# Kernel tuning notes

Hardware: AMD Instinct MI355X
Metric: run time of the kernel (lower is better)

## Reference

```python
import jax, jax.numpy as jnp
import numpy as np

B, D, C, H, L = 32768, 64, 64, 1024, 6
EPS = 1e-5
NIN = (D - D // 2) + C  # unchanged half + cond = 96
SPLIT = D // 2          # 32


def setup_inputs() -> dict:
    key = jax.random.key(0)
    ks = jax.random.split(key, 12)
    s = 0.05
    return {
        "z": jax.random.normal(ks[0], (B, D), jnp.float32),
        "cond": jax.random.normal(ks[1], (B, C), jnp.float32),
        "W1": jax.random.normal(ks[2], (L, NIN, H), jnp.float32) * s,
        "b1": jax.random.normal(ks[3], (L, H), jnp.float32) * s,
        "W2": jax.random.normal(ks[4], (L, H, H), jnp.float32) * s,
        "b2": jax.random.normal(ks[5], (L, H), jnp.float32) * s,
        "Ws": jax.random.normal(ks[6], (L, H, SPLIT), jnp.float32) * s,
        "bs": jax.random.normal(ks[7], (L, SPLIT), jnp.float32) * s,
        "Wt": jax.random.normal(ks[8], (L, H, SPLIT), jnp.float32) * s,
        "bt": jax.random.normal(ks[9], (L, SPLIT), jnp.float32) * s,
        "bn_w": 1.0 + 0.1 * jax.random.normal(ks[10], (L, D), jnp.float32),
        "bn_b": 0.1 * jax.random.normal(ks[11], (L, D), jnp.float32),
    }


def reference(z, cond, W1, b1, W2, b2, Ws, bs, Wt, bt, bn_w, bn_b):
    x = z
    log_det = jnp.zeros((z.shape[0],), z.dtype)
    for i in range(L):
        # 'even' mask keeps even indices on even layers, odd indices otherwise
        if i % 2 == 0:
            keep, chg = np.arange(0, D, 2), np.arange(1, D, 2)
        else:
            keep, chg = np.arange(1, D, 2), np.arange(0, D, 2)
        # 2-layer MLP on [x_keep, cond]
        h = jax.nn.relu(jnp.concatenate([x[:, keep], cond], axis=1) @ W1[i] + b1[i])
        h = jax.nn.relu(h @ W2[i] + b2[i])
        log_s = jnp.tanh(h @ Ws[i] + bs[i])          # (B, SPLIT)
        t = h @ Wt[i] + bt[i]                         # (B, SPLIT)
        x2t = x[:, chg] * jnp.exp(log_s) + t
        x = jnp.zeros_like(x).at[:, keep].set(x[:, keep]).at[:, chg].set(x2t)
        log_det = log_det + log_s.sum(axis=1)
        # BatchNorm1d, training mode: batch mean / biased variance, eps=1e-5
        mean = x.mean(axis=0)
        var = x.var(axis=0)
        x = (x - mean) * jax.lax.rsqrt(var + EPS) * bn_w[i] + bn_b[i]
        log_det = log_det + jnp.log(jnp.abs(bn_w[i])).sum()
    return x, log_det
```

## Files before the change

kernel.cpp:

```cpp
#include <hip/hip_runtime.h>
#include <math.h>

#define BB 32768
#define DD 64
#define CC 64
#define HH 1024
#define LL 6
#define SPLIT 32
#define NIN 96
#define EPSV 1e-5f

typedef short short8 __attribute__((ext_vector_type(8)));
typedef float f32x4 __attribute__((ext_vector_type(4)));
typedef unsigned short u16;

__device__ __forceinline__ u16 f2bf(float f) {
    union { float f; unsigned int u; } c; c.f = f;
    unsigned int u = c.u + 0x7FFFu + ((c.u >> 16) & 1u);
    return (u16)(u >> 16);
}

__device__ __forceinline__ void gl_lds16(const u16* g, u16* l) {
    __builtin_amdgcn_global_load_lds(
        (const __attribute__((address_space(1))) unsigned int*)g,
        (__attribute__((address_space(3))) unsigned int*)l, 16, 0, 0);
}

__global__ void transpose_cvt_kernel(const float* __restrict__ src, u16* __restrict__ dst,
                                     int R, int C, int Rpad,
                                     long long sstride, long long dstride)
{
    __shared__ float tile[32][33];
    const float* s = src + (size_t)blockIdx.z * sstride;
    u16* d = dst + (size_t)blockIdx.z * dstride;
    int r0 = blockIdx.x * 32, c0 = blockIdx.y * 32;
    int tc = threadIdx.x & 31, tr = threadIdx.x >> 5;
#pragma unroll
    for (int i = 0; i < 4; ++i) {
        int r = r0 + tr + i * 8;
        tile[tr + i * 8][tc] = (r < R) ? s[(size_t)r * C + c0 + tc] : 0.f;
    }
    __syncthreads();
#pragma unroll
    for (int i = 0; i < 4; ++i) {
        int cc = tr + i * 8;
        d[(size_t)(c0 + cc) * Rpad + r0 + tc] = f2bf(tile[tc][cc]);
    }
}

__global__ __launch_bounds__(256)
void init_ain_cond_kernel(const float* __restrict__ cond, u16* __restrict__ Ain)
{
    int t = blockIdx.x * 256 + threadIdx.x;
    int c = t % 96, r = t / 96;
    Ain[(size_t)r * 128 + 32 + c] = (c < CC) ? f2bf(cond[(size_t)r * CC + c]) : (u16)0;
}

__global__ __launch_bounds__(256)
void build_keep_kernel(const float* __restrict__ x, u16* __restrict__ Ain, int keep_off)
{
    int t = blockIdx.x * 256 + threadIdx.x;
    int c = t & 31, r = t >> 5;
    Ain[(size_t)r * 128 + c] = f2bf(x[(size_t)r * DD + 2 * c + keep_off]);
}

__global__ __launch_bounds__(512, 4)
void gemm_tiled(const u16* __restrict__ A,
                const u16* __restrict__ Bt,
                const float* __restrict__ bias,
                u16* __restrict__ Cc,
                int K)
{
    __shared__ u16 sA[3][8 * 512];
    __shared__ u16 sB[3][16 * 512];

    const int t = threadIdx.x;
    const int w = t >> 6, lane = t & 63;
    const int lane16 = lane & 15, quad = lane >> 4;
    const int wm = w >> 2, wn = w & 3;

    int id = blockIdx.x;
    int nby = gridDim.x >> 2;
    int xcd = id & 7, slot = id >> 3;
    int bx = slot & 3, byq = slot >> 2;
    int by = xcd * (nby >> 3) + byq;
    const int bm = by * 128, bn = bx * 256;

    const int niter = K >> 5;

    auto stage = [&](int it, int buf) {
        int k0 = it * 32;
#pragma unroll
        for (int e3 = 0; e3 < 3; ++e3) {
            int e = w + e3 * 8;
            if (e < 8) {
                const u16* g = A + (size_t)(bm + e * 16 + lane16) * K + k0 + quad * 8;
                gl_lds16(g, &sA[buf][e * 512]);
            } else {
                int j = e - 8;
                const u16* g = Bt + (size_t)(bn + j * 16 + lane16) * K + k0 + quad * 8;
                gl_lds16(g, &sB[buf][j * 512]);
            }
        }
    };

    f32x4 acc[4][4];
#pragma unroll
    for (int a = 0; a < 4; ++a)
#pragma unroll
        for (int b = 0; b < 4; ++b) acc[a][b] = (f32x4){0.f, 0.f, 0.f, 0.f};

    const unsigned sAb = (unsigned)(size_t)(__attribute__((address_space(3))) u16*)&sA[0][0];
    const unsigned sBb = (unsigned)(size_t)(__attribute__((address_space(3))) u16*)&sB[0][0];
    const unsigned aoff = (unsigned)(wm * 4096 + lane * 16);
    const unsigned boff = (unsigned)(wn * 4096 + lane * 16);

    stage(0, 0);
    stage(1, 1);
    int buf = 0, sbuf = 2;
    for (int it = 0; it < niter; ++it) {
        asm volatile("s_waitcnt vmcnt(3)");
        __builtin_amdgcn_s_barrier();

        const unsigned aA = sAb + (unsigned)(buf * 8192)  + aoff;
        const unsigned aB = sBb + (unsigned)(buf * 16384) + boff;
        short8 af0, af1, af2, af3, bf0, bf1, bf2, bf3;
        asm volatile("ds_read_b128 %0, %1 offset:0"    : "=v"(af0) : "v"(aA));
        asm volatile("ds_read_b128 %0, %1 offset:1024" : "=v"(af1) : "v"(aA));
        asm volatile("ds_read_b128 %0, %1 offset:2048" : "=v"(af2) : "v"(aA));
        asm volatile("ds_read_b128 %0, %1 offset:3072" : "=v"(af3) : "v"(aA));
        asm volatile("ds_read_b128 %0, %1 offset:0"    : "=v"(bf0) : "v"(aB));
        asm volatile("ds_read_b128 %0, %1 offset:1024" : "=v"(bf1) : "v"(aB));
        asm volatile("ds_read_b128 %0, %1 offset:2048" : "=v"(bf2) : "v"(aB));
        asm volatile("ds_read_b128 %0, %1 offset:3072" : "=v"(bf3) : "v"(aB));

        if (it + 2 < niter)        stage(it + 2, sbuf);
        else if (it + 2 == niter)  stage(niter - 1, sbuf);

        asm volatile("s_waitcnt lgkmcnt(0)");
        __builtin_amdgcn_sched_barrier(0);

        short8 af[4] = {af0, af1, af2, af3};
        short8 bfr[4] = {bf0, bf1, bf2, bf3};
#pragma unroll
        for (int a = 0; a < 4; ++a)
#pragma unroll
            for (int b = 0; b < 4; ++b)
                acc[a][b] = __builtin_amdgcn_mfma_f32_16x16x32_bf16(af[a], bfr[b], acc[a][b], 0, 0, 0);

        buf  = (buf  == 2) ? 0 : buf  + 1;
        sbuf = (sbuf == 2) ? 0 : sbuf + 1;
    }
    __syncthreads();

    constexpr int ES = 72;
    float bv[4];
#pragma unroll
    for (int b = 0; b < 4; ++b) bv[b] = bias[bn + wn * 64 + b * 16 + lane16];
    u16* scr = ((u16*)sB) + w * (16 * ES);
#pragma unroll
    for (int a = 0; a < 4; ++a) {
#pragma unroll
        for (int b = 0; b < 4; ++b)
#pragma unroll
            for (int r = 0; r < 4; ++r) {
                float v = fmaxf(acc[a][b][r] + bv[b], 0.f);
                scr[(quad * 4 + r) * ES + b * 16 + lane16] = f2bf(v);
            }
#pragma unroll
        for (int ch = 0; ch < 2; ++ch) {
            int row = ch * 8 + (lane >> 3), colc = (lane & 7) * 8;
            short8 v = *(const short8*)(scr + row * ES + colc);
            *(short8*)(Cc + (size_t)(bm + wm * 64 + a * 16 + row) * 1024 + bn + wn * 64 + colc) = v;
        }
    }
}

__global__ __launch_bounds__(512)
void gemm3_coupling(const u16* __restrict__ A,
                    const u16* __restrict__ Bt,
                    const float* __restrict__ bs, const float* __restrict__ bt,
                    float* __restrict__ x, float* __restrict__ log_det,
                    float* __restrict__ stat_sum, float* __restrict__ stat_sumsq,
                    int keep_off, int row0)
{
    constexpr int ST_STRIDE = 66;
    __shared__ u16 stg[2][24 * 512];
    __shared__ float ssum[8][64], ssum2[8][64];
    float* sst = (float*)stg;

    const int t = threadIdx.x;
    const int w = t >> 6, lane = t & 63;
    const int lane16 = lane & 15, quad = lane >> 4;
    const int wm = w >> 1, wn = w & 1;
    const int bm = blockIdx.x * 128;

    auto stage = [&](int it, int buf) {
        int k0 = it * 64;
#pragma unroll
        for (int p = 0; p < 3; ++p) {
            int e = w + p * 8;
            if (e < 16) {
                int s = e >> 3, i = e & 7;
                const u16* g = A + (size_t)(bm + i * 16 + lane16) * HH + (k0 + s * 32 + quad * 8);
                gl_lds16(g, &stg[buf][e * 512]);
            } else {
                int j2 = e - 16, s = j2 >> 2, j = j2 & 3;
                const u16* g = Bt + (size_t)(j * 16 + lane16) * HH + (k0 + s * 32 + quad * 8);
                gl_lds16(g, &stg[buf][e * 512]);
            }
        }
    };

    f32x4 acc[2][2];
#pragma unroll
    for (int a = 0; a < 2; ++a)
#pragma unroll
        for (int b = 0; b < 2; ++b) acc[a][b] = (f32x4){0.f, 0.f, 0.f, 0.f};

    stage(0, 0);
    for (int it = 0; it < 16; ++it) {
        const int buf = it & 1;
        __syncthreads();
        if (it + 1 < 16) stage(it + 1, buf ^ 1);
        u16* ldsA = stg[buf];
        u16* ldsB = stg[buf] + 16 * 512;
#pragma unroll
        for (int s = 0; s < 2; ++s) {
            short8 af[2], bfr[2];
#pragma unroll
            for (int a = 0; a < 2; ++a)
                af[a] = *(const short8*)(ldsA + ((s * 8 + wm * 2 + a) * 512) + lane * 8);
#pragma unroll
            for (int b = 0; b < 2; ++b)
                bfr[b] = *(const short8*)(ldsB + ((s * 4 + wn * 2 + b) * 512) + lane * 8);
#pragma unroll
            for (int a = 0; a < 2; ++a)
#pragma unroll
                for (int b = 0; b < 2; ++b)
                    acc[a][b] = __builtin_amdgcn_mfma_f32_16x16x32_bf16(af[a], bfr[b], acc[a][b], 0, 0, 0);
        }
    }
    __syncthreads();

#pragma unroll
    for (int a = 0; a < 2; ++a)
#pragma unroll
        for (int b = 0; b < 2; ++b)
#pragma unroll
            for (int r = 0; r < 4; ++r) {
                int row = wm * 32 + a * 16 + quad * 4 + r;
                int col = wn * 32 + b * 16 + lane16;
                sst[row * ST_STRIDE + col] = acc[a][b][r];
            }
    __syncthreads();

    const int f = lane;
    const bool is_chg = ((f & 1) != keep_off);
    const int j = f >> 1;
    float bsj = 0.f, btj = 0.f;
    if (is_chg) { bsj = bs[j]; btj = bt[j]; }

    float lsum = 0.f, lsum2 = 0.f;
    for (int i = 0; i < 16; ++i) {
        int crow = w * 16 + i;
        int grow = row0 + bm + crow;
        float xv = x[(size_t)grow * DD + f];
        float ld = 0.f;
        if (is_chg) {
            float s_raw = sst[crow * ST_STRIDE + j];
            float t_raw = sst[crow * ST_STRIDE + SPLIT + j];
            float ls = tanhf(s_raw + bsj);
            float tv = t_raw + btj;
            xv = xv * expf(ls) + tv;
            x[(size_t)grow * DD + f] = xv;
            ld = ls;
        }
        for (int off = 32; off > 0; off >>= 1) ld += __shfl_down(ld, off, 64);
        if (f == 0) log_det[grow] += ld;
        lsum  += xv;
        lsum2 += xv * xv;
    }

    ssum[w][f]  = lsum;
    ssum2[w][f] = lsum2;
    __syncthreads();
    if (t < 64) {
        float a = 0.f, b = 0.f;
#pragma unroll
        for (int g = 0; g < 8; ++g) { a += ssum[g][t]; b += ssum2[g][t]; }
        atomicAdd(stat_sum + t, a);
        atomicAdd(stat_sumsq + t, b);
    }
}

__global__ __launch_bounds__(256)
void normalize_kernel(const float* __restrict__ xin, float* __restrict__ xout,
                      const float* __restrict__ stat_sum, const float* __restrict__ stat_sumsq,
                      const float* __restrict__ bn_w, const float* __restrict__ bn_b,
                      float* __restrict__ log_det,
                      u16* __restrict__ Ain, int off_next)
{
    __shared__ float sscale[64], sshift[64], scsum;
    int t = threadIdx.x;
    if (t < 64) {
        const float invB = 1.f / (float)BB;
        float mean = stat_sum[t] * invB;
        float var  = stat_sumsq[t] * invB - mean * mean;
        float inv  = rsqrtf(var + EPSV);
        float wv   = bn_w[t];
        float sc   = inv * wv;
        sscale[t] = sc;
        sshift[t] = bn_b[t] - mean * sc;
        float lg = logf(fabsf(wv));
        for (int off = 32; off > 0; off >>= 1) lg += __shfl_down(lg, off, 64);
        if (t == 0) scsum = lg;
    }
    __syncthreads();

    int idx = blockIdx.x * blockDim.x + t;
    int f0 = (idx & 15) * 4;
    int row = idx >> 4;
    float4 v = ((const float4*)xin)[idx];
    v.x = v.x * sscale[f0 + 0] + sshift[f0 + 0];
    v.y = v.y * sscale[f0 + 1] + sshift[f0 + 1];
    v.z = v.z * sscale[f0 + 2] + sshift[f0 + 2];
    v.w = v.w * sscale[f0 + 3] + sshift[f0 + 3];
    ((float4*)xout)[idx] = v;
    if ((idx & 15) == 0) log_det[row] += scsum;
    if (Ain) {
        float a0 = off_next ? v.y : v.x;
        float a1 = off_next ? v.w : v.z;
        ushort2 u; u.x = f2bf(a0); u.y = f2bf(a1);
        *(ushort2*)(Ain + (size_t)row * 128 + (f0 >> 1)) = u;
    }
}

extern "C" void kernel_launch(void* const* d_in, const int* in_sizes, int n_in,
                              void* d_out, int out_size, void* d_ws, size_t ws_size,
                              hipStream_t stream)
{
    const float* z    = (const float*)d_in[0];
    const float* cond = (const float*)d_in[1];
    const float* W1   = (const float*)d_in[2];
    const float* b1   = (const float*)d_in[3];
    const float* W2   = (const float*)d_in[4];
    const float* b2   = (const float*)d_in[5];
    const float* Ws   = (const float*)d_in[6];
    const float* bs   = (const float*)d_in[7];
    const float* Wt   = (const float*)d_in[8];
    const float* bt   = (const float*)d_in[9];
    const float* bn_w = (const float*)d_in[10];
    const float* bn_b = (const float*)d_in[11];

    float* out_x  = (float*)d_out;
    float* out_ld = out_x + (size_t)BB * DD;

    char* p = (char*)d_ws;
    size_t used = 0;
    auto alloc = [&](size_t bytes) { void* q = p + used; used += (bytes + 255) & ~(size_t)255; return q; };

    float* xbuf = (float*)alloc((size_t)BB * DD * 4);
    u16*   w1t  = (u16*)alloc((size_t)LL * HH * 128 * 2);
    u16*   w2t  = (u16*)alloc((size_t)LL * HH * HH * 2);
    u16*   wstt = (u16*)alloc((size_t)LL * 64 * HH * 2);
    u16*   Ain  = (u16*)alloc((size_t)BB * 128 * 2);
    float* stat_sum   = (float*)alloc(64 * 4);
    float* stat_sumsq = (float*)alloc(64 * 4);

    int CH = BB;
    while (CH > 8192 && used + (size_t)CH * 4096 + 4096 > ws_size) CH >>= 1;
    u16* h1 = (u16*)alloc((size_t)CH * HH * 2);
    u16* h2 = (u16*)alloc((size_t)CH * HH * 2);

    hipMemcpyAsync(xbuf, z, (size_t)BB * DD * sizeof(float), hipMemcpyDeviceToDevice, stream);
    hipMemsetAsync(out_ld, 0, (size_t)BB * sizeof(float), stream);

    transpose_cvt_kernel<<<dim3(128/32, HH/32, LL), 256, 0, stream>>>(
        W1, w1t, NIN, HH, 128, (long long)NIN * HH, (long long)HH * 128);
    transpose_cvt_kernel<<<dim3(HH/32, HH/32, LL), 256, 0, stream>>>(
        W2, w2t, HH, HH, HH, (long long)HH * HH, (long long)HH * HH);
    transpose_cvt_kernel<<<dim3(HH/32, SPLIT/32, LL), 256, 0, stream>>>(
        Ws, wstt, HH, SPLIT, HH, (long long)HH * SPLIT, (long long)64 * HH);
    transpose_cvt_kernel<<<dim3(HH/32, SPLIT/32, LL), 256, 0, stream>>>(
        Wt, wstt + (size_t)SPLIT * HH, HH, SPLIT, HH, (long long)HH * SPLIT, (long long)64 * HH);

    init_ain_cond_kernel<<<BB * 96 / 256, 256, 0, stream>>>(cond, Ain);
    build_keep_kernel<<<BB * 32 / 256, 256, 0, stream>>>(xbuf, Ain, 0);

    for (int l = 0; l < LL; ++l) {
        const int off = l & 1;
        hipMemsetAsync(stat_sum, 0, 2 * 64 * sizeof(float), stream);

        for (int c = 0; c < BB / CH; ++c) {
            const int row0 = c * CH;

            gemm_tiled<<<(CH / 128) * 4, 512, 0, stream>>>(
                Ain + (size_t)row0 * 128, w1t + (size_t)l * HH * 128,
                b1 + (size_t)l * HH, h1, 128);

            gemm_tiled<<<(CH / 128) * 4, 512, 0, stream>>>(
                h1, w2t + (size_t)l * HH * HH,
                b2 + (size_t)l * HH, h2, HH);

            gemm3_coupling<<<CH / 128, 512, 0, stream>>>(
                h2, wstt + (size_t)l * 64 * HH,
                bs + (size_t)l * SPLIT, bt + (size_t)l * SPLIT,
                xbuf, out_ld, stat_sum, stat_sumsq, off, row0);
        }

        float* xout = (l == LL - 1) ? out_x : xbuf;
        u16* ain_next = (l < LL - 1) ? Ain : nullptr;
        normalize_kernel<<<(BB * DD / 4) / 256, 256, 0, stream>>>(
            xbuf, xout, stat_sum, stat_sumsq,
            bn_w + (size_t)l * DD, bn_b + (size_t)l * DD,
            out_ld, ain_next, (l + 1) & 1);
    }
}
```

Measured before the change: 1.088 ms.

## Enlarge GEMM block tile to 256x256 and split MFMA issue around LDS reads

The main bf16 GEMM block tile grows from 128x256 to 256x256, so each wave computes a 128x64 sub-tile with 32 accumulators, which raises the arithmetic done per staged A/B byte. The K-loop now waits for only the first half of its LDS fragment reads before issuing half of the MFMAs, and raises wave priority around the MFMA bursts. The cost is higher register and LDS use, with launch bounds lowered to 2 blocks per CU, and half as many blocks per chunk, which may leave CUs underused when chunks are small.

```diff
diff --git a/kernel.cpp b/kernel.cpp
--- a/kernel.cpp
+++ b/kernel.cpp
@@ -64,14 +64,14 @@
     Ain[(size_t)r * 128 + c] = f2bf(x[(size_t)r * DD + 2 * c + keep_off]);
 }
 
-__global__ __launch_bounds__(512, 4)
+__global__ __launch_bounds__(512, 2)
 void gemm_tiled(const u16* __restrict__ A,
                 const u16* __restrict__ Bt,
                 const float* __restrict__ bias,
                 u16* __restrict__ Cc,
                 int K)
 {
-    __shared__ u16 sA[3][8 * 512];
+    __shared__ u16 sA[3][16 * 512];
     __shared__ u16 sB[3][16 * 512];
 
     const int t = threadIdx.x;
@@ -84,69 +84,81 @@
     int xcd = id & 7, slot = id >> 3;
     int bx = slot & 3, byq = slot >> 2;
     int by = xcd * (nby >> 3) + byq;
-    const int bm = by * 128, bn = bx * 256;
+    const int bm = by * 256, bn = bx * 256;
 
     const int niter = K >> 5;
 
     auto stage = [&](int it, int buf) {
         int k0 = it * 32;
 #pragma unroll
-        for (int e3 = 0; e3 < 3; ++e3) {
-            int e = w + e3 * 8;
-            if (e < 8) {
+        for (int p = 0; p < 4; ++p) {
+            int e = w + (p & 1) * 8;
+            if (p < 2) {
                 const u16* g = A + (size_t)(bm + e * 16 + lane16) * K + k0 + quad * 8;
                 gl_lds16(g, &sA[buf][e * 512]);
             } else {
-                int j = e - 8;
-                const u16* g = Bt + (size_t)(bn + j * 16 + lane16) * K + k0 + quad * 8;
-                gl_lds16(g, &sB[buf][j * 512]);
+                const u16* g = Bt + (size_t)(bn + e * 16 + lane16) * K + k0 + quad * 8;
+                gl_lds16(g, &sB[buf][e * 512]);
             }
         }
     };
 
-    f32x4 acc[4][4];
-#pragma unroll
-    for (int a = 0; a < 4; ++a)
+    f32x4 acc[8][4];
+#pragma unroll
+    for (int a = 0; a < 8; ++a)
 #pragma unroll
         for (int b = 0; b < 4; ++b) acc[a][b] = (f32x4){0.f, 0.f, 0.f, 0.f};
 
     const unsigned sAb = (unsigned)(size_t)(__attribute__((address_space(3))) u16*)&sA[0][0];
     const unsigned sBb = (unsigned)(size_t)(__attribute__((address_space(3))) u16*)&sB[0][0];
-    const unsigned aoff = (unsigned)(wm * 4096 + lane * 16);
+    const unsigned aoff = (unsigned)(wm * 8192 + lane * 16);
     const unsigned boff = (unsigned)(wn * 4096 + lane * 16);
 
     stage(0, 0);
     stage(1, 1);
     int buf = 0, sbuf = 2;
     for (int it = 0; it < niter; ++it) {
-        asm volatile("s_waitcnt vmcnt(3)");
+        asm volatile("s_waitcnt vmcnt(4)");
         __builtin_amdgcn_s_barrier();
 
-        const unsigned aA = sAb + (unsigned)(buf * 8192)  + aoff;
+        const unsigned aA = sAb + (unsigned)(buf * 16384) + aoff;
         const unsigned aB = sBb + (unsigned)(buf * 16384) + boff;
-        short8 af0, af1, af2, af3, bf0, bf1, bf2, bf3;
-        asm volatile("ds_read_b128 %0, %1 offset:0"    : "=v"(af0) : "v"(aA));
-        asm volatile("ds_read_b128 %0, %1 offset:1024" : "=v"(af1) : "v"(aA));
-        asm volatile("ds_read_b128 %0, %1 offset:2048" : "=v"(af2) : "v"(aA));
-        asm volatile("ds_read_b128 %0, %1 offset:3072" : "=v"(af3) : "v"(aA));
-        asm volatile("ds_read_b128 %0, %1 offset:0"    : "=v"(bf0) : "v"(aB));
-        asm volatile("ds_read_b128 %0, %1 offset:1024" : "=v"(bf1) : "v"(aB));
-        asm volatile("ds_read_b128 %0, %1 offset:2048" : "=v"(bf2) : "v"(aB));
-        asm volatile("ds_read_b128 %0, %1 offset:3072" : "=v"(bf3) : "v"(aB));
+        short8 af[8], bf[4];
+        asm volatile("ds_read_b128 %0, %1 offset:0"    : "=v"(bf[0]) : "v"(aB));
+        asm volatile("ds_read_b128 %0, %1 offset:1024" : "=v"(bf[1]) : "v"(aB));
+        asm volatile("ds_read_b128 %0, %1 offset:2048" : "=v"(bf[2]) : "v"(aB));
+        asm volatile("ds_read_b128 %0, %1 offset:3072" : "=v"(bf[3]) : "v"(aB));
+        asm volatile("ds_read_b128 %0, %1 offset:0"    : "=v"(af[0]) : "v"(aA));
+        asm volatile("ds_read_b128 %0, %1 offset:1024" : "=v"(af[1]) : "v"(aA));
+        asm volatile("ds_read_b128 %0, %1 offset:2048" : "=v"(af[2]) : "v"(aA));
+        asm volatile("ds_read_b128 %0, %1 offset:3072" : "=v"(af[3]) : "v"(aA));
+        asm volatile("ds_read_b128 %0, %1 offset:4096" : "=v"(af[4]) : "v"(aA));
+        asm volatile("ds_read_b128 %0, %1 offset:5120" : "=v"(af[5]) : "v"(aA));
+        asm volatile("ds_read_b128 %0, %1 offset:6144" : "=v"(af[6]) : "v"(aA));
+        asm volatile("ds_read_b128 %0, %1 offset:7168" : "=v"(af[7]) : "v"(aA));
 
         if (it + 2 < niter)        stage(it + 2, sbuf);
         else if (it + 2 == niter)  stage(niter - 1, sbuf);
 
+        asm volatile("s_waitcnt lgkmcnt(4)");
+        __builtin_amdgcn_sched_barrier(0);
+        __builtin_amdgcn_s_setprio(1);
+#pragma unroll
+        for (int a = 0; a < 4; ++a)
+#pragma unroll
+            for (int b = 0; b < 4; ++b)
+                acc[a][b] = __builtin_amdgcn_mfma_f32_16x16x32_bf16(af[a], bf[b], acc[a][b], 0, 0, 0);
+        __builtin_amdgcn_s_setprio(0);
+
         asm volatile("s_waitcnt lgkmcnt(0)");
         __builtin_amdgcn_sched_barrier(0);
-
-        short8 af[4] = {af0, af1, af2, af3};
-        short8 bfr[4] = {bf0, bf1, bf2, bf3};
-#pragma unroll
-        for (int a = 0; a < 4; ++a)
+        __builtin_amdgcn_s_setprio(1);
+#pragma unroll
+        for (int a = 4; a < 8; ++a)
 #pragma unroll
             for (int b = 0; b < 4; ++b)
-                acc[a][b] = __builtin_amdgcn_mfma_f32_16x16x32_bf16(af[a], bfr[b], acc[a][b], 0, 0, 0);
+                acc[a][b] = __builtin_amdgcn_mfma_f32_16x16x32_bf16(af[a], bf[b], acc[a][b], 0, 0, 0);
+        __builtin_amdgcn_s_setprio(0);
 
         buf  = (buf  == 2) ? 0 : buf  + 1;
         sbuf = (sbuf == 2) ? 0 : sbuf + 1;
@@ -159,7 +171,7 @@
     for (int b = 0; b < 4; ++b) bv[b] = bias[bn + wn * 64 + b * 16 + lane16];
     u16* scr = ((u16*)sB) + w * (16 * ES);
 #pragma unroll
-    for (int a = 0; a < 4; ++a) {
+    for (int a = 0; a < 8; ++a) {
 #pragma unroll
         for (int b = 0; b < 4; ++b)
 #pragma unroll
@@ -171,7 +183,7 @@
         for (int ch = 0; ch < 2; ++ch) {
             int row = ch * 8 + (lane >> 3), colc = (lane & 7) * 8;
             short8 v = *(const short8*)(scr + row * ES + colc);
-            *(short8*)(Cc + (size_t)(bm + wm * 64 + a * 16 + row) * 1024 + bn + wn * 64 + colc) = v;
+            *(short8*)(Cc + (size_t)(bm + wm * 128 + a * 16 + row) * 1024 + bn + wn * 64 + colc) = v;
         }
     }
 }
@@ -395,11 +407,11 @@
         for (int c = 0; c < BB / CH; ++c) {
             const int row0 = c * CH;
 
-            gemm_tiled<<<(CH / 128) * 4, 512, 0, stream>>>(
+            gemm_tiled<<<(CH / 256) * 4, 512, 0, stream>>>(
                 Ain + (size_t)row0 * 128, w1t + (size_t)l * HH * 128,
                 b1 + (size_t)l * HH, h1, 128);
 
-            gemm_tiled<<<(CH / 128) * 4, 512, 0, stream>>>(
+            gemm_tiled<<<(CH / 256) * 4, 512, 0, stream>>>(
                 h1, w2t + (size_t)l * HH * HH,
                 b2 + (size_t)l * HH, h2, HH);
 
```

Measured after the change: 952.7 us. -12.4%, faster.
